# Optimization experiments

Measured on AMD Instinct MI355X. Metric: run time of the kernel, lower is better.

Reference implementation:

```python
import jax, jax.numpy as jnp
import numpy as np

B, C, H, L = 8, 1, 512, 4096


def setup_inputs() -> dict:
    key = jax.random.key(0)
    k1, k2, k3, k4, k5 = jax.random.split(key, 5)
    u = jax.random.normal(k1, (B, H, L), dtype=jnp.float32)
    # SSM kernel k (C, H, L): stand-in for HippoSSKernel output, scaled so the
    # length-L convolution has O(1) variance.
    k = jax.random.normal(k2, (C, H, L), dtype=jnp.float32) * (1.0 / np.sqrt(L))
    D = jax.random.normal(k3, (C, H), dtype=jnp.float32)
    # output_linear: pointwise linear (C*H) -> H
    W = jax.random.normal(k4, (H, C * H), dtype=jnp.float32) * (1.0 / np.sqrt(C * H))
    b = jax.random.normal(k5, (H,), dtype=jnp.float32) * 0.01
    return {"u": u, "k": k, "D": D, "W": W, "b": b}


def reference(u, k, D, W, b):
    # u: (B, H, L), k: (C, H, L), D: (C, H), W: (H, C*H), b: (H,)
    Lq = u.shape[-1]
    n = 2 * Lq  # zero-padded FFT length for linear (non-circular) convolution
    k_f = jnp.fft.rfft(k, n=n)                       # (C, H, n//2+1) complex
    u_f = jnp.fft.rfft(u, n=n)                       # (B, H, n//2+1) complex
    y_f = jnp.einsum('bhl,chl->bchl', u_f, k_f)      # freq-domain multiply
    y = jnp.fft.irfft(y_f, n=n)[..., :Lq]            # (B, C, H, L)
    y = y + jnp.einsum('bhl,ch->bchl', u, D)         # skip term
    Bq, Cq, Hq, _ = y.shape
    y = y.reshape(Bq, Cq * Hq, Lq)                   # (B, C*H, L)
    y = jax.nn.gelu(y, approximate=False)            # torch GELU (erf)
    y = jnp.einsum('bcl,dc->bdl', y, W) + b[None, :, None]  # pointwise linear
    return y
```

## Files before the change

### kernel.cpp

```cpp
#include <hip/hip_runtime.h>
#include <hip/hip_bf16.h>
#include <math.h>

#define L_DIM 4096
#define H_DIM 512
#define B_DIM 8
#define SEG 2048

typedef __attribute__((ext_vector_type(8))) short short8;
typedef __attribute__((ext_vector_type(4))) float floatx4;

__device__ __forceinline__ unsigned f2bf(float f) {
    unsigned x = __float_as_uint(f);
    return (x + 0x7fffu + ((x >> 16) & 1u)) >> 16;
}

__global__ __launch_bounds__(512, 6) void conv_gelu_mfma(
    const float* __restrict__ u,
    const float* __restrict__ kk,
    const float* __restrict__ Dp,
    unsigned short* __restrict__ g,
    const float* __restrict__ W,
    unsigned short* __restrict__ Wb)
{
    __shared__ __align__(16) unsigned short kA[4144];
    __shared__ __align__(16) unsigned short kB[4144];
    __shared__ __align__(16) unsigned short us[8][2104];

    const int h   = blockIdx.x;
    const int Lb  = blockIdx.y << 11;
    const int tid = threadIdx.x;
    const int lane = tid & 63;
    const int w   = tid >> 6;
    const int i   = lane & 15;
    const int q   = lane >> 4;
    const int b   = i & 7;
    const int s   = i >> 3;

    if (Wb != nullptr && blockIdx.y == 0) {
        const float* wsrc = W + (size_t)h * H_DIM;
        unsigned short* wdst = Wb + (size_t)h * H_DIM;
        wdst[tid] = (unsigned short)f2bf(wsrc[tid]);
    }

    const float* kh = kk + (size_t)h * L_DIM;

    for (int p = tid; p < 4144; p += 512) {
        int t1 = L_DIM + 15 - p;
        int t2 = L_DIM + 14 - p;
        float v1 = (t1 >= 0 && t1 < L_DIM) ? kh[t1] : 0.0f;
        float v2 = (t2 >= 0 && t2 < L_DIM) ? kh[t2] : 0.0f;
        kA[p] = (unsigned short)f2bf(v1);
        kB[p] = (unsigned short)f2bf(v2);
    }

    floatx4 acc[8];
    #pragma unroll
    for (int t = 0; t < 8; t++) acc[t] = (floatx4){0.f, 0.f, 0.f, 0.f};

    const char* kbase = (const char*)((i & 1) ? kA : kB);
    const int aconst = 2 * (L_DIM + ((i & 1) ? 15 : 14) - i + 8 * q);
    const int basew = Lb + 32 * w;

    union AFrag { int x[4]; short8 v; };

    for (int seg = 0; seg < 2; seg++) {
        const int ms = seg * SEG;
        const int mstart = (seg == 0) ? -32 : SEG;
        const int segmax = ms + SEG - 32;
        if (seg == 1) {
            if (Lb + 2016 < SEG) break;
            __syncthreads();
        }
        for (int e = tid * 4; e < 2096; e += 2048) {
            int m = ms - 32 + e;
            #pragma unroll
            for (int bb = 0; bb < 8; bb++) {
                float4 v = make_float4(0.f, 0.f, 0.f, 0.f);
                if (m >= 0 && m < L_DIM)
                    v = *(const float4*)(u + ((size_t)bb * H_DIM + h) * L_DIM + m);
                unsigned lo = f2bf(v.x) | (f2bf(v.y) << 16);
                unsigned hi = f2bf(v.z) | (f2bf(v.w) << 16);
                *(uint2*)&us[bb][e] = make_uint2(lo, hi);
            }
        }
        __syncthreads();

        const char* bbase = (const char*)&us[b][0] + 2 * (32 - ms + 16 * s + 8 * q);
        const char* ab = kbase + aconst;

        for (int c = 0; c < 8; c++) {
            const int c32 = 32 * c;
            const int rel = basew - c32;
            const int j_hi = (rel - mstart) >> 8;
            int j_lo = (rel - segmax + 255) >> 8;
            if (j_lo < -7) j_lo = -7;
            if (j_hi < j_lo) continue;
            const int n = j_hi - j_lo + 1;

            AFrag Wd[8];
            #pragma unroll
            for (int d = 1; d < 8; d++) {
                const int dd = c32 + (j_hi + d) * 256;
                if (dd >= 0) {
                    const int* ap = (const int*)(ab - 2 * dd);
                    Wd[d].x[0] = ap[0]; Wd[d].x[1] = ap[1];
                    Wd[d].x[2] = ap[2]; Wd[d].x[3] = ap[3];
                } else {
                    Wd[d].x[0] = 0; Wd[d].x[1] = 0; Wd[d].x[2] = 0; Wd[d].x[3] = 0;
                }
            }

            const char* aab = ab - 2 * c32 - 512 * j_hi;
            const char* bb0 = bbase + 2 * (rel - 256 * j_hi);

            for (int jb = 0; jb < n; jb += 8) {
                #pragma unroll
                for (int k = 0; k < 8; k++) {
                    const int jj = jb + k;
                    if (jj < n) {
                        const int dd0 = c32 + (j_hi - jj) * 256;
                        AFrag nf;
                        if (dd0 >= 0) {
                            const int* ap = (const int*)(aab + 512 * jj);
                            nf.x[0] = ap[0]; nf.x[1] = ap[1];
                            nf.x[2] = ap[2]; nf.x[3] = ap[3];
                        } else {
                            nf.x[0] = 0; nf.x[1] = 0; nf.x[2] = 0; nf.x[3] = 0;
                        }
                        Wd[(8 - k) & 7] = nf;
                        short8 bf = *(const short8*)(bb0 + 512 * jj);
                        #pragma unroll
                        for (int t = 0; t < 8; t++)
                            acc[t] = __builtin_amdgcn_mfma_f32_16x16x32_bf16(
                                Wd[(t - k) & 7].v, bf, acc[t], 0, 0, 0);
                    }
                }
            }
        }
    }

    const float Dh = Dp[h];
    #pragma unroll
    for (int t = 0; t < 8; t++) {
        const int l0 = Lb + 32 * w + 256 * t;
        const int lb2 = l0 + 16 * s + 4 * q;
        const size_t off = ((size_t)b * H_DIM + h) * L_DIM + lb2;
        float4 uv = *(const float4*)(u + off);
        float y0 = acc[t][0] + uv.x * Dh;
        float y1 = acc[t][1] + uv.y * Dh;
        float y2 = acc[t][2] + uv.z * Dh;
        float y3 = acc[t][3] + uv.w * Dh;
        const float c = 0.70710678118654752f;
        float g0 = 0.5f * y0 * (1.0f + erff(y0 * c));
        float g1 = 0.5f * y1 * (1.0f + erff(y1 * c));
        float g2 = 0.5f * y2 * (1.0f + erff(y2 * c));
        float g3 = 0.5f * y3 * (1.0f + erff(y3 * c));
        unsigned lo = f2bf(g0) | (f2bf(g1) << 16);
        unsigned hi = f2bf(g2) | (f2bf(g3) << 16);
        *(uint2*)(g + off) = make_uint2(lo, hi);
    }
}

template <bool PREW>
__global__ __launch_bounds__(512, 4) void pointwise_mfma(
    const unsigned short* __restrict__ g,
    const unsigned short* __restrict__ Wb,
    const float* __restrict__ W,
    const float* __restrict__ bias,
    float* __restrict__ out)
{
    __shared__ __align__(16) unsigned gs2[2][128 * 40];
    __shared__ __align__(16) unsigned short ws[2][128 * 76];

    const int tid = threadIdx.x;
    const int d0 = blockIdx.x * 128;
    const int l0 = blockIdx.y * 128;
    const int bz = blockIdx.z;
    const int w  = tid >> 6;
    const int lane = tid & 63;
    const int n  = lane & 15;
    const int q  = lane >> 4;
    const int wh = w & 1;
    const int wd = w >> 1;

    const int p   = tid & 31;
    const int oct = (tid >> 5) & 7;
    const int hi  = tid >> 8;

    const int quarter = tid & 3;
    const int rb      = tid >> 2;

    floatx4 acc[4][2];
    #pragma unroll
    for (int mt = 0; mt < 4; mt++)
        #pragma unroll
        for (int nt = 0; nt < 2; nt++) acc[mt][nt] = (floatx4){0.f, 0.f, 0.f, 0.f};

    const unsigned short* gbase = g + ((size_t)bz * H_DIM + 2 * p) * L_DIM + l0 + 16 * oct + 8 * hi;

    uint4 ga, gb, wa, wb;

    auto LOAD = [&](int c0) {
        const unsigned short* gp = gbase + (size_t)c0 * L_DIM;
        ga = *(const uint4*)gp;
        gb = *(const uint4*)(gp + L_DIM);
        if (PREW) {
            const unsigned short* wp = Wb + (size_t)(d0 + rb) * H_DIM + c0 + 16 * quarter;
            wa = ((const uint4*)wp)[0];
            wb = ((const uint4*)wp)[1];
        } else {
            const float* wp = W + (size_t)(d0 + rb) * H_DIM + c0 + 16 * quarter;
            float4 f0 = ((const float4*)wp)[0];
            float4 f1 = ((const float4*)wp)[1];
            float4 f2 = ((const float4*)wp)[2];
            float4 f3 = ((const float4*)wp)[3];
            wa = make_uint4(f2bf(f0.x) | (f2bf(f0.y) << 16), f2bf(f0.z) | (f2bf(f0.w) << 16),
                            f2bf(f1.x) | (f2bf(f1.y) << 16), f2bf(f1.z) | (f2bf(f1.w) << 16));
            wb = make_uint4(f2bf(f2.x) | (f2bf(f2.y) << 16), f2bf(f2.z) | (f2bf(f2.w) << 16),
                            f2bf(f3.x) | (f2bf(f3.y) << 16), f2bf(f3.z) | (f2bf(f3.w) << 16));
        }
    };
    auto WRITE = [&](int bf) {
        const unsigned* ua = (const unsigned*)&ga;
        const unsigned* ub = (const unsigned*)&gb;
        #pragma unroll
        for (int e = 0; e < 4; e++) {
            unsigned w0 = (ua[e] & 0xFFFFu) | (ub[e] << 16);
            unsigned w1 = (ua[e] >> 16) | (ub[e] & 0xFFFF0000u);
            const int lrow = 16 * oct + 8 * hi + 2 * e;
            gs2[bf][lrow * 40 + p] = w0;
            gs2[bf][(lrow + 1) * 40 + p] = w1;
        }
        *(uint4*)&ws[bf][rb * 76 + 16 * quarter]     = wa;
        *(uint4*)&ws[bf][rb * 76 + 16 * quarter + 8] = wb;
    };

    LOAD(0);
    WRITE(0);
    __syncthreads();

    for (int it = 0; it < 8; it++) {
        const int cur = it & 1;
        if (it < 7) LOAD(64 * (it + 1));
        #pragma unroll
        for (int ks = 0; ks < 2; ks++) {
            short8 bfr[2];
            #pragma unroll
            for (int nt = 0; nt < 2; nt++)
                bfr[nt] = *(const short8*)&ws[cur][(32 * wd + 16 * nt + n) * 76 + 32 * ks + 8 * q];
            #pragma unroll
            for (int mt = 0; mt < 4; mt++) {
                union { uint4 u4; short8 v; } af;
                af.u4 = *(const uint4*)&gs2[cur][(64 * wh + 16 * mt + n) * 40 + 16 * ks + 4 * q];
                #pragma unroll
                for (int nt = 0; nt < 2; nt++)
                    acc[mt][nt] = __builtin_amdgcn_mfma_f32_16x16x32_bf16(af.v, bfr[nt], acc[mt][nt], 0, 0, 0);
            }
        }
        if (it < 7) WRITE(cur ^ 1);
        __syncthreads();
    }

    #pragma unroll
    for (int nt = 0; nt < 2; nt++) {
        const int d = d0 + 32 * wd + 16 * nt + n;
        const float bb = bias[d];
        float* obase = out + ((size_t)bz * H_DIM + d) * L_DIM + l0 + 64 * wh + 4 * q;
        #pragma unroll
        for (int mt = 0; mt < 4; mt++) {
            float4 r = make_float4(acc[mt][nt][0] + bb, acc[mt][nt][1] + bb,
                                   acc[mt][nt][2] + bb, acc[mt][nt][3] + bb);
            *(float4*)(obase + 16 * mt) = r;
        }
    }
}

extern "C" void kernel_launch(void* const* d_in, const int* in_sizes, int n_in,
                              void* d_out, int out_size, void* d_ws, size_t ws_size,
                              hipStream_t stream) {
    const float* u    = (const float*)d_in[0];
    const float* k    = (const float*)d_in[1];
    const float* D    = (const float*)d_in[2];
    const float* W    = (const float*)d_in[3];
    const float* bias = (const float*)d_in[4];
    float* out = (float*)d_out;
    unsigned short* g = (unsigned short*)d_ws;

    const size_t g_bytes = (size_t)B_DIM * H_DIM * L_DIM * sizeof(unsigned short);
    const size_t w_bytes = (size_t)H_DIM * H_DIM * sizeof(unsigned short);
    const bool prew = ws_size >= g_bytes + w_bytes;
    unsigned short* Wb = prew ? (unsigned short*)((char*)d_ws + g_bytes) : nullptr;

    conv_gelu_mfma<<<dim3(H_DIM, L_DIM / 2048), 512, 0, stream>>>(u, k, D, g, W, Wb);
    if (prew)
        pointwise_mfma<true><<<dim3(H_DIM / 128, L_DIM / 128, B_DIM), 512, 0, stream>>>(g, Wb, W, bias, out);
    else
        pointwise_mfma<false><<<dim3(H_DIM / 128, L_DIM / 128, B_DIM), 512, 0, stream>>>(g, nullptr, W, bias, out);
}
```

Before: 248.2 us.

## Enlarge pointwise GEMM tile and read pre-swizzled weights straight from global

The first kernel now writes the bf16 copy of W in MFMA-fragment order, so the pointwise kernel can load B operands directly from global memory or cache. That removes the weight staging in LDS and its shared-memory stores. The pointwise kernel moves to 256x256 tiles with 1024 threads and a 4x4 accumulator grid per wave, so each g tile is re-read fewer times across output-channel tiles. The cost is only 256 blocks, which gives less parallelism and latency hiding, plus more accumulator register pressure and uncached-looking weight loads inside the inner loop.

```diff
diff --git a/kernel.cpp b/kernel.cpp
--- a/kernel.cpp
+++ b/kernel.cpp
@@ -39,8 +39,9 @@
 
     if (Wb != nullptr && blockIdx.y == 0) {
         const float* wsrc = W + (size_t)h * H_DIM;
-        unsigned short* wdst = Wb + (size_t)h * H_DIM;
-        wdst[tid] = (unsigned short)f2bf(wsrc[tid]);
+        const int c = tid;
+        const int idx = (((h >> 4) * 64 + (c >> 3)) * 16 + (h & 15)) * 8 + (c & 7);
+        Wb[idx] = (unsigned short)f2bf(wsrc[c]);
     }
 
     const float* kh = kk + (size_t)h * L_DIM;
@@ -163,63 +164,43 @@
 }
 
 template <bool PREW>
-__global__ __launch_bounds__(512, 4) void pointwise_mfma(
+__global__ __launch_bounds__(1024, 4) void pointwise_mfma(
     const unsigned short* __restrict__ g,
     const unsigned short* __restrict__ Wb,
     const float* __restrict__ W,
     const float* __restrict__ bias,
     float* __restrict__ out)
 {
-    __shared__ __align__(16) unsigned gs2[2][128 * 40];
-    __shared__ __align__(16) unsigned short ws[2][128 * 76];
+    __shared__ __align__(16) unsigned gs2[2][256 * 40];
 
     const int tid = threadIdx.x;
-    const int d0 = blockIdx.x * 128;
-    const int l0 = blockIdx.y * 128;
+    const int d0 = blockIdx.x * 256;
+    const int l0 = blockIdx.y * 256;
     const int bz = blockIdx.z;
     const int w  = tid >> 6;
     const int lane = tid & 63;
     const int n  = lane & 15;
     const int q  = lane >> 4;
-    const int wh = w & 1;
-    const int wd = w >> 1;
+    const int wl = w >> 2;
+    const int wd = w & 3;
 
     const int p   = tid & 31;
-    const int oct = (tid >> 5) & 7;
-    const int hi  = tid >> 8;
-
-    const int quarter = tid & 3;
-    const int rb      = tid >> 2;
-
-    floatx4 acc[4][2];
+    const int grp = tid >> 5;
+
+    floatx4 acc[4][4];
     #pragma unroll
     for (int mt = 0; mt < 4; mt++)
         #pragma unroll
-        for (int nt = 0; nt < 2; nt++) acc[mt][nt] = (floatx4){0.f, 0.f, 0.f, 0.f};
-
-    const unsigned short* gbase = g + ((size_t)bz * H_DIM + 2 * p) * L_DIM + l0 + 16 * oct + 8 * hi;
-
-    uint4 ga, gb, wa, wb;
+        for (int nt = 0; nt < 4; nt++) acc[mt][nt] = (floatx4){0.f, 0.f, 0.f, 0.f};
+
+    const unsigned short* gbase = g + ((size_t)bz * H_DIM + 2 * p) * L_DIM + l0 + 8 * grp;
+
+    uint4 ga, gb;
 
     auto LOAD = [&](int c0) {
         const unsigned short* gp = gbase + (size_t)c0 * L_DIM;
         ga = *(const uint4*)gp;
         gb = *(const uint4*)(gp + L_DIM);
-        if (PREW) {
-            const unsigned short* wp = Wb + (size_t)(d0 + rb) * H_DIM + c0 + 16 * quarter;
-            wa = ((const uint4*)wp)[0];
-            wb = ((const uint4*)wp)[1];
-        } else {
-            const float* wp = W + (size_t)(d0 + rb) * H_DIM + c0 + 16 * quarter;
-            float4 f0 = ((const float4*)wp)[0];
-            float4 f1 = ((const float4*)wp)[1];
-            float4 f2 = ((const float4*)wp)[2];
-            float4 f3 = ((const float4*)wp)[3];
-            wa = make_uint4(f2bf(f0.x) | (f2bf(f0.y) << 16), f2bf(f0.z) | (f2bf(f0.w) << 16),
-                            f2bf(f1.x) | (f2bf(f1.y) << 16), f2bf(f1.z) | (f2bf(f1.w) << 16));
-            wb = make_uint4(f2bf(f2.x) | (f2bf(f2.y) << 16), f2bf(f2.z) | (f2bf(f2.w) << 16),
-                            f2bf(f3.x) | (f2bf(f3.y) << 16), f2bf(f3.z) | (f2bf(f3.w) << 16));
-        }
     };
     auto WRITE = [&](int bf) {
         const unsigned* ua = (const unsigned*)&ga;
@@ -228,12 +209,10 @@
         for (int e = 0; e < 4; e++) {
             unsigned w0 = (ua[e] & 0xFFFFu) | (ub[e] << 16);
             unsigned w1 = (ua[e] >> 16) | (ub[e] & 0xFFFF0000u);
-            const int lrow = 16 * oct + 8 * hi + 2 * e;
+            const int lrow = 8 * grp + 2 * e;
             gs2[bf][lrow * 40 + p] = w0;
             gs2[bf][(lrow + 1) * 40 + p] = w1;
         }
-        *(uint4*)&ws[bf][rb * 76 + 16 * quarter]     = wa;
-        *(uint4*)&ws[bf][rb * 76 + 16 * quarter + 8] = wb;
     };
 
     LOAD(0);
@@ -242,31 +221,50 @@
 
     for (int it = 0; it < 8; it++) {
         const int cur = it & 1;
+        const int c0 = 64 * it;
         if (it < 7) LOAD(64 * (it + 1));
+
         #pragma unroll
         for (int ks = 0; ks < 2; ks++) {
-            short8 bfr[2];
-            #pragma unroll
-            for (int nt = 0; nt < 2; nt++)
-                bfr[nt] = *(const short8*)&ws[cur][(32 * wd + 16 * nt + n) * 76 + 32 * ks + 8 * q];
+            short8 bw[4];
+            #pragma unroll
+            for (int nt = 0; nt < 4; nt++) {
+                if (PREW) {
+                    const unsigned short* wp = Wb +
+                        ((((size_t)(d0 >> 4) + 4 * wd + nt) * 64 + (c0 >> 3) + 4 * ks + q) * 16 + n) * 8;
+                    bw[nt] = *(const short8*)wp;
+                } else {
+                    const int d = d0 + 64 * wd + 16 * nt + n;
+                    const float* wp = W + (size_t)d * H_DIM + c0 + 32 * ks + 8 * q;
+                    float4 f0 = ((const float4*)wp)[0];
+                    float4 f1 = ((const float4*)wp)[1];
+                    union { unsigned u[4]; short8 v; } pk;
+                    pk.u[0] = f2bf(f0.x) | (f2bf(f0.y) << 16);
+                    pk.u[1] = f2bf(f0.z) | (f2bf(f0.w) << 16);
+                    pk.u[2] = f2bf(f1.x) | (f2bf(f1.y) << 16);
+                    pk.u[3] = f2bf(f1.z) | (f2bf(f1.w) << 16);
+                    bw[nt] = pk.v;
+                }
+            }
             #pragma unroll
             for (int mt = 0; mt < 4; mt++) {
                 union { uint4 u4; short8 v; } af;
-                af.u4 = *(const uint4*)&gs2[cur][(64 * wh + 16 * mt + n) * 40 + 16 * ks + 4 * q];
+                af.u4 = *(const uint4*)&gs2[cur][(64 * wl + 16 * mt + n) * 40 + 16 * ks + 4 * q];
                 #pragma unroll
-                for (int nt = 0; nt < 2; nt++)
-                    acc[mt][nt] = __builtin_amdgcn_mfma_f32_16x16x32_bf16(af.v, bfr[nt], acc[mt][nt], 0, 0, 0);
-            }
-        }
+                for (int nt = 0; nt < 4; nt++)
+                    acc[mt][nt] = __builtin_amdgcn_mfma_f32_16x16x32_bf16(af.v, bw[nt], acc[mt][nt], 0, 0, 0);
+            }
+        }
+
         if (it < 7) WRITE(cur ^ 1);
         __syncthreads();
     }
 
     #pragma unroll
-    for (int nt = 0; nt < 2; nt++) {
-        const int d = d0 + 32 * wd + 16 * nt + n;
+    for (int nt = 0; nt < 4; nt++) {
+        const int d = d0 + 64 * wd + 16 * nt + n;
         const float bb = bias[d];
-        float* obase = out + ((size_t)bz * H_DIM + d) * L_DIM + l0 + 64 * wh + 4 * q;
+        float* obase = out + ((size_t)bz * H_DIM + d) * L_DIM + l0 + 64 * wl + 4 * q;
         #pragma unroll
         for (int mt = 0; mt < 4; mt++) {
             float4 r = make_float4(acc[mt][nt][0] + bb, acc[mt][nt][1] + bb,
@@ -294,7 +292,7 @@
 
     conv_gelu_mfma<<<dim3(H_DIM, L_DIM / 2048), 512, 0, stream>>>(u, k, D, g, W, Wb);
     if (prew)
-        pointwise_mfma<true><<<dim3(H_DIM / 128, L_DIM / 128, B_DIM), 512, 0, stream>>>(g, Wb, W, bias, out);
+        pointwise_mfma<true><<<dim3(H_DIM / 256, L_DIM / 256, B_DIM), 1024, 0, stream>>>(g, Wb, W, bias, out);
     else
-        pointwise_mfma<false><<<dim3(H_DIM / 128, L_DIM / 128, B_DIM), 512, 0, stream>>>(g, nullptr, W, bias, out);
-}
+        pointwise_mfma<false><<<dim3(H_DIM / 256, L_DIM / 256, B_DIM), 1024, 0, stream>>>(g, nullptr, W, bias, out);
+}
```

New measurement: 239.8 us. 1.03x faster.
